# Performance work log

Hardware: AMD Instinct MI355X
Metric: run time of the kernel (lower is better)

The kernel has to match this reference:

```python
import jax, jax.numpy as jnp
import numpy as np

N = 100000    # nodes
E = 1600000   # edges (avg degree 16)
IN = 128      # input feature dim
D = 32        # per-head hidden dim
H = 4         # heads for hidden layers
C = 16        # num_classes (final per-head dim)
NEG = 0.2     # leaky_relu negative slope


def setup_inputs() -> dict:
    key = jax.random.key(0)
    ks = jax.random.split(key, 14)
    s = jnp.float32(0.05)
    f32 = jnp.float32
    inp = {
        "inputs": jax.random.normal(ks[0], (N, IN), f32),
        "src": jax.random.randint(ks[1], (E,), 0, N),
        "dst": jax.random.randint(ks[2], (E,), 0, N),
        # layer 0: IN -> (H, D), no residual
        "W0": jax.random.normal(ks[3], (IN, H * D), f32) * s,
        "al0": jax.random.normal(ks[4], (H, D), f32) * s,
        "ar0": jax.random.normal(ks[5], (H, D), f32) * s,
        # layer 1: H*D -> (H, D), identity residual (dims match)
        "W1": jax.random.normal(ks[6], (H * D, H * D), f32) * s,
        "al1": jax.random.normal(ks[7], (H, D), f32) * s,
        "ar1": jax.random.normal(ks[8], (H, D), f32) * s,
        # final layer: H*D -> (1, C), linear residual projection
        "W2": jax.random.normal(ks[9], (H * D, 1 * C), f32) * s,
        "al2": jax.random.normal(ks[10], (1, C), f32) * s,
        "ar2": jax.random.normal(ks[11], (1, C), f32) * s,
        "resW2": jax.random.normal(ks[12], (H * D, 1 * C), f32) * s,
    }
    return inp


def gat_conv(h, W, al, ar, src, dst, n_heads, out_dim, res=None, act=None):
    # h: (N, F_in) -> out: (N, n_heads, out_dim)
    feat = (h @ W).reshape(N, n_heads, out_dim)            # (N,H,D)
    el = jnp.sum(feat * al, axis=-1)                       # (N,H)
    er = jnp.sum(feat * ar, axis=-1)                       # (N,H)
    e = jax.nn.leaky_relu(el[src] + er[dst], NEG)          # (E,H)
    # softmax over incoming edges per destination node
    emax = jax.ops.segment_max(e, dst, num_segments=N)     # (N,H)
    ex = jnp.exp(e - emax[dst])                            # (E,H)
    den = jax.ops.segment_sum(ex, dst, num_segments=N)     # (N,H)
    alpha = ex / den[dst]                                  # (E,H)
    msg = feat[src] * alpha[:, :, None]                    # (E,H,D) -- dominant traffic
    out = jax.ops.segment_sum(msg, dst, num_segments=N)    # (N,H,D)
    if res is not None:
        out = out + res
    if act is not None:
        out = act(out)
    return out


def reference(inputs, src, dst, W0, al0, ar0, W1, al1, ar1, W2, al2, ar2, resW2):
    # hidden layer 0 (no residual), GATConv activation = elu, then flatten + relu
    h = gat_conv(inputs, W0, al0, ar0, src, dst, H, D, res=None, act=jax.nn.elu)
    h = jax.nn.relu(h.reshape(N, H * D))
    # hidden layer 1, identity residual (in == H*D)
    res1 = h.reshape(N, H, D)
    h = gat_conv(h, W1, al1, ar1, src, dst, H, D, res=res1, act=jax.nn.elu)
    h = jax.nn.relu(h.reshape(N, H * D))
    # output layer: 1 head, linear residual projection, no activation, mean over heads
    res2 = (h @ resW2).reshape(N, 1, C)
    out = gat_conv(h, W2, al2, ar2, src, dst, 1, C, res=res2, act=None)
    return out.mean(axis=1)                                # (N, C)
```

## Files before the change

kernel.cpp:

```cpp
#include <hip/hip_runtime.h>

#define N_NODES 100000
#define N_EDGES 1600000
#define IN_F    128
#define NEG_SLOPE 0.2f
#define NBUCK   512
#define PCHUNK  4096

typedef __attribute__((ext_vector_type(8))) short bf16x8;
typedef __attribute__((ext_vector_type(4))) float f32x4;

__device__ __forceinline__ float bf2f(unsigned short u) {
    return __uint_as_float(((unsigned int)u) << 16);
}

__device__ __forceinline__ unsigned short f2bf(float f) {
    unsigned int u = __float_as_uint(f);
    u += 0x7FFFu + ((u >> 16) & 1u);
    return (unsigned short)(u >> 16);
}

__global__ __launch_bounds__(256) void pack_w128(const float* __restrict__ W,
                                                 unsigned short* __restrict__ Wp) {
    int idx = blockIdx.x * 256 + threadIdx.x;
    int j  = idx & 7;
    int l  = (idx >> 3) & 63;
    int kt = (idx >> 9) & 3;
    int nt = idx >> 11;
    int k  = kt * 32 + (l >> 4) * 8 + j;
    int n  = nt * 16 + (l & 15);
    Wp[idx] = f2bf(W[k * 128 + n]);
}

__global__ __launch_bounds__(256) void pack_w32(const float* __restrict__ W2,
                                                const float* __restrict__ rW2,
                                                unsigned short* __restrict__ Wp) {
    int idx = blockIdx.x * 256 + threadIdx.x;
    int j  = idx & 7;
    int l  = (idx >> 3) & 63;
    int kt = (idx >> 9) & 3;
    int nt = idx >> 11;
    int k  = kt * 32 + (l >> 4) * 8 + j;
    int n  = nt * 16 + (l & 15);
    float v = (n < 16) ? W2[k * 16 + n] : rW2[k * 16 + (n - 16)];
    Wp[idx] = f2bf(v);
}

__global__ __launch_bounds__(256) void gemm128_mfma(const float* __restrict__ A,
                                                    const unsigned short* __restrict__ Wp,
                                                    const float* __restrict__ al,
                                                    const float* __restrict__ ar,
                                                    unsigned short* __restrict__ featb,
                                                    float* __restrict__ el,
                                                    float* __restrict__ er,
                                                    int nrows) {
    __shared__ unsigned short sA[64][136];
    const int t    = threadIdx.x;
    const int row0 = blockIdx.x * 64;

#pragma unroll
    for (int i = 0; i < 8; ++i) {
        int e  = (i * 256 + t) * 4;
        int r  = e >> 7;
        int c  = e & 127;
        float4 v = make_float4(0.f, 0.f, 0.f, 0.f);
        int gr = row0 + r;
        if (gr < nrows) v = *(const float4*)(A + (size_t)gr * IN_F + c);
        ushort4 u;
        u.x = f2bf(v.x); u.y = f2bf(v.y); u.z = f2bf(v.z); u.w = f2bf(v.w);
        *(ushort4*)(&sA[r][c]) = u;
    }
    __syncthreads();

    const int wv   = t >> 6;
    const int lane = t & 63;
    const int q    = lane >> 4;
    const int m    = lane & 15;
    const int m0   = wv * 16;

    f32x4 acc[8];
#pragma unroll
    for (int nt = 0; nt < 8; ++nt) acc[nt] = (f32x4){0.f, 0.f, 0.f, 0.f};

#pragma unroll
    for (int kt = 0; kt < 4; ++kt) {
        bf16x8 afr = *(const bf16x8*)(&sA[m0 + m][kt * 32 + q * 8]);
#pragma unroll
        for (int nt = 0; nt < 8; ++nt) {
            bf16x8 bfr = *(const bf16x8*)(Wp + ((size_t)(nt * 4 + kt) * 64 + lane) * 8);
            acc[nt] = __builtin_amdgcn_mfma_f32_16x16x32_bf16(afr, bfr, acc[nt], 0, 0, 0);
        }
    }

    float pel[16], per[16];
#pragma unroll
    for (int i = 0; i < 16; ++i) { pel[i] = 0.f; per[i] = 0.f; }

#pragma unroll
    for (int nt = 0; nt < 8; ++nt) {
        const int col = nt * 16 + m;
        const float alv = al[col];
        const float arv = ar[col];
        const int h = nt >> 1;
#pragma unroll
        for (int reg = 0; reg < 4; ++reg) {
            int row = row0 + m0 + q * 4 + reg;
            float a = acc[nt][reg];
            if (row < nrows) featb[(size_t)row * 128 + col] = f2bf(a);
            pel[reg * 4 + h] += a * alv;
            per[reg * 4 + h] += a * arv;
        }
    }

#pragma unroll
    for (int s = 8; s > 0; s >>= 1) {
#pragma unroll
        for (int i = 0; i < 16; ++i) {
            pel[i] += __shfl_down(pel[i], s);
            per[i] += __shfl_down(per[i], s);
        }
    }
    if (m == 0) {
#pragma unroll
        for (int reg = 0; reg < 4; ++reg) {
            int row = row0 + m0 + q * 4 + reg;
            if (row < nrows) {
#pragma unroll
                for (int h = 0; h < 4; ++h) {
                    el[row * 4 + h] = pel[reg * 4 + h];
                    er[row * 4 + h] = per[reg * 4 + h];
                }
            }
        }
    }
}

__global__ __launch_bounds__(256) void gemm16_mfma(const float* __restrict__ A,
                                                   const unsigned short* __restrict__ Wp,
                                                   const float* __restrict__ al,
                                                   const float* __restrict__ ar,
                                                   unsigned short* __restrict__ feat2b,
                                                   float* __restrict__ res2,
                                                   float* __restrict__ el,
                                                   float* __restrict__ er,
                                                   int nrows) {
    __shared__ unsigned short sA[64][136];
    const int t    = threadIdx.x;
    const int row0 = blockIdx.x * 64;

#pragma unroll
    for (int i = 0; i < 8; ++i) {
        int e  = (i * 256 + t) * 4;
        int r  = e >> 7;
        int c  = e & 127;
        float4 v = make_float4(0.f, 0.f, 0.f, 0.f);
        int gr = row0 + r;
        if (gr < nrows) v = *(const float4*)(A + (size_t)gr * IN_F + c);
        ushort4 u;
        u.x = f2bf(v.x); u.y = f2bf(v.y); u.z = f2bf(v.z); u.w = f2bf(v.w);
        *(ushort4*)(&sA[r][c]) = u;
    }
    __syncthreads();

    const int wv   = t >> 6;
    const int lane = t & 63;
    const int q    = lane >> 4;
    const int m    = lane & 15;
    const int m0   = wv * 16;

    f32x4 acc0 = (f32x4){0.f, 0.f, 0.f, 0.f};
    f32x4 acc1 = (f32x4){0.f, 0.f, 0.f, 0.f};

#pragma unroll
    for (int kt = 0; kt < 4; ++kt) {
        bf16x8 afr = *(const bf16x8*)(&sA[m0 + m][kt * 32 + q * 8]);
        bf16x8 b0  = *(const bf16x8*)(Wp + ((size_t)(0 * 4 + kt) * 64 + lane) * 8);
        bf16x8 b1  = *(const bf16x8*)(Wp + ((size_t)(1 * 4 + kt) * 64 + lane) * 8);
        acc0 = __builtin_amdgcn_mfma_f32_16x16x32_bf16(afr, b0, acc0, 0, 0, 0);
        acc1 = __builtin_amdgcn_mfma_f32_16x16x32_bf16(afr, b1, acc1, 0, 0, 0);
    }

    float pel[4], per[4];
    const float alv = al[m];
    const float arv = ar[m];
#pragma unroll
    for (int reg = 0; reg < 4; ++reg) {
        int row = row0 + m0 + q * 4 + reg;
        float a = acc0[reg];
        if (row < nrows) {
            feat2b[(size_t)row * 16 + m] = f2bf(a);
            res2[(size_t)row * 16 + m]   = acc1[reg];
        }
        pel[reg] = a * alv;
        per[reg] = a * arv;
    }
#pragma unroll
    for (int s = 8; s > 0; s >>= 1) {
#pragma unroll
        for (int reg = 0; reg < 4; ++reg) {
            pel[reg] += __shfl_down(pel[reg], s);
            per[reg] += __shfl_down(per[reg], s);
        }
    }
    if (m == 0) {
#pragma unroll
        for (int reg = 0; reg < 4; ++reg) {
            int row = row0 + m0 + q * 4 + reg;
            if (row < nrows) { el[row] = pel[reg]; er[row] = per[reg]; }
        }
    }
}

__global__ __launch_bounds__(256) void bucket_count_k(const int* __restrict__ dst,
                                                      int* __restrict__ bcount, int nE) {
    __shared__ int hist[NBUCK];
    const int t = threadIdx.x;
    hist[t] = 0; hist[t + 256] = 0;
    __syncthreads();
    const int start = blockIdx.x * PCHUNK;
#pragma unroll
    for (int j = 0; j < PCHUNK / 256; ++j) {
        int e = start + j * 256 + t;
        if (e < nE) atomicAdd(&hist[dst[e] >> 8], 1);
    }
    __syncthreads();
    if (hist[t])       atomicAdd(&bcount[t],       hist[t]);
    if (hist[t + 256]) atomicAdd(&bcount[t + 256], hist[t + 256]);
}

__global__ __launch_bounds__(NBUCK) void scan512(const int* __restrict__ bcount,
                                                 int* __restrict__ bbase,
                                                 int* __restrict__ bcursor) {
    __shared__ int s[NBUCK];
    const int t = threadIdx.x;
    int v = bcount[t];
    s[t] = v;
    __syncthreads();
#pragma unroll
    for (int off = 1; off < NBUCK; off <<= 1) {
        int x = (t >= off) ? s[t - off] : 0;
        __syncthreads();
        s[t] += x;
        __syncthreads();
    }
    int excl = s[t] - v;
    bbase[t]   = excl;
    bcursor[t] = excl;
}

__global__ __launch_bounds__(512) void partition_k(const int* __restrict__ src,
                                                   const int* __restrict__ dst,
                                                   int* __restrict__ bcursor,
                                                   uint2* __restrict__ pe, int nE) {
    __shared__ int   hist[NBUCK];
    __shared__ int   lstart[NBUCK];
    __shared__ int   gbase[NBUCK];
    __shared__ int   curB[NBUCK];
    __shared__ uint2 reorder[PCHUNK];

    const int t = threadIdx.x;
    const int start = blockIdx.x * PCHUNK;
    const int m = min(PCHUNK, nE - start);

    hist[t] = 0;
    __syncthreads();

#pragma unroll
    for (int j = 0; j < PCHUNK / 512; ++j) {
        int e = start + j * 512 + t;
        if (e < nE) atomicAdd(&hist[dst[e] >> 8], 1);
    }
    __syncthreads();
    const int cnt = hist[t];

    __shared__ int s[NBUCK];
    s[t] = cnt;
    __syncthreads();
#pragma unroll
    for (int off = 1; off < NBUCK; off <<= 1) {
        int x = (t >= off) ? s[t - off] : 0;
        __syncthreads();
        s[t] += x;
        __syncthreads();
    }
    lstart[t] = s[t] - cnt;
    curB[t]   = s[t] - cnt;
    gbase[t] = cnt ? atomicAdd(&bcursor[t], cnt) : 0;
    __syncthreads();

#pragma unroll
    for (int j = 0; j < PCHUNK / 512; ++j) {
        int e = start + j * 512 + t;
        if (e < nE) {
            int d = dst[e];
            int pos = atomicAdd(&curB[d >> 8], 1);
            reorder[pos] = make_uint2((unsigned)src[e], (unsigned)d);
        }
    }
    __syncthreads();

    for (int i = t; i < m; i += 512) {
        uint2 ed = reorder[i];
        int b = (int)(ed.y >> 8);
        pe[gbase[b] + (i - lstart[b])] = ed;
    }
}

__global__ __launch_bounds__(256) void bucket_finalize(const uint2* __restrict__ pe,
                                                       const int* __restrict__ bbase,
                                                       int* __restrict__ rowptr,
                                                       int* __restrict__ deg,
                                                       int* __restrict__ sorted_src,
                                                       int nE) {
    __shared__ int deg_l[256];
    __shared__ int s[256];
    __shared__ int cur[256];

    const int b  = blockIdx.x;
    const int t  = threadIdx.x;
    const int base = bbase[b];
    const int endE = (b + 1 < NBUCK) ? bbase[b + 1] : nE;
    const int cnt  = endE - base;
    const int n    = b * 256 + t;

    deg_l[t] = 0;
    __syncthreads();
    for (int i = t; i < cnt; i += 256)
        atomicAdd(&deg_l[pe[base + i].y & 255u], 1);
    __syncthreads();

    const int dv = deg_l[t];
    s[t] = dv;
    __syncthreads();
#pragma unroll
    for (int off = 1; off < 256; off <<= 1) {
        int x = (t >= off) ? s[t - off] : 0;
        __syncthreads();
        s[t] += x;
        __syncthreads();
    }
    const int off_l = s[t] - dv;
    if (n < N_NODES) {
        rowptr[n] = base + off_l;
        deg[n]    = dv;
    }
    cur[t] = off_l;
    __syncthreads();

    for (int i = t; i < cnt; i += 256) {
        uint2 ed = pe[base + i];
        int pos = atomicAdd(&cur[ed.y & 255u], 1);
        sorted_src[base + pos] = (int)ed.x;
    }
}

__global__ __launch_bounds__(256) void gat_agg128(const int* __restrict__ rowptr,
                                                  const int* __restrict__ deg,
                                                  const int* __restrict__ sorted_src,
                                                  const float* __restrict__ el,
                                                  const float* __restrict__ er,
                                                  const unsigned short* __restrict__ featb,
                                                  const float* __restrict__ res,
                                                  float* __restrict__ out) {
    __shared__ int   sS[4][64];
    __shared__ float sW[4][64][4];

    const int wv   = threadIdx.x >> 6;
    const int lane = threadIdx.x & 63;
    const int nd   = blockIdx.x * 4 + wv;

    const int dg = deg[nd];
    const int r0 = rowptr[nd];
    const int h  = lane >> 4;
    const float4 er4 = *(const float4*)(er + nd * 4);

    float den = 0.f;
    float ax = 0.f, ay = 0.f;

    for (int base = 0; base < dg; base += 64) {
        int m = dg - base; if (m > 64) m = 64;
        if (lane < m) {
            int s = sorted_src[r0 + base + lane];
            sS[wv][lane] = s;
            float4 e4 = *(const float4*)(el + s * 4);
            float4 w;
            float v;
            v = e4.x + er4.x; v = v > 0.f ? v : NEG_SLOPE * v; w.x = __expf(v);
            v = e4.y + er4.y; v = v > 0.f ? v : NEG_SLOPE * v; w.y = __expf(v);
            v = e4.z + er4.z; v = v > 0.f ? v : NEG_SLOPE * v; w.z = __expf(v);
            v = e4.w + er4.w; v = v > 0.f ? v : NEG_SLOPE * v; w.w = __expf(v);
            *(float4*)(&sW[wv][lane][0]) = w;
        }
        for (int i = 0; i < m; ++i) {
            int s   = sS[wv][i];
            float w = sW[wv][i][h];
            den += w;
            ushort2 u = *(const ushort2*)(featb + (size_t)s * 128 + lane * 2);
            ax += w * bf2f(u.x);
            ay += w * bf2f(u.y);
        }
    }

    float scale = den > 0.f ? 1.f / den : 0.f;
    float ox = ax * scale, oy = ay * scale;
    size_t o0 = (size_t)nd * 128 + lane * 2;
    if (res) { ox += res[o0]; oy += res[o0 + 1]; }
    ox = fmaxf(ox, 0.f);
    oy = fmaxf(oy, 0.f);
    *(float2*)(out + o0) = make_float2(ox, oy);
}

__global__ __launch_bounds__(256) void gat_agg16(const int* __restrict__ rowptr,
                                                 const int* __restrict__ deg,
                                                 const int* __restrict__ sorted_src,
                                                 const float* __restrict__ el,
                                                 const float* __restrict__ er,
                                                 const unsigned short* __restrict__ feat2b,
                                                 const float* __restrict__ res,
                                                 float* __restrict__ out) {
    __shared__ int   sS[4][64];
    __shared__ float sW[4][64];

    const int wv   = threadIdx.x >> 6;
    const int lane = threadIdx.x & 63;
    const int nd   = blockIdx.x * 4 + wv;
    const int g    = lane >> 3;
    const int f2   = (lane & 7) * 2;

    const int dg = deg[nd];
    const int r0 = rowptr[nd];
    const float erd = er[nd];

    float ax = 0.f, ay = 0.f, den = 0.f;

    for (int base = 0; base < dg; base += 64) {
        int m = dg - base; if (m > 64) m = 64;
        if (lane < m) {
            int s = sorted_src[r0 + base + lane];
            sS[wv][lane] = s;
            float v = el[s] + erd;
            v = v > 0.f ? v : NEG_SLOPE * v;
            sW[wv][lane] = __expf(v);
        }
        for (int i = g; i < m; i += 8) {
            int s   = sS[wv][i];
            float w = sW[wv][i];
            den += w;
            ushort2 u = *(const ushort2*)(feat2b + (size_t)s * 16 + f2);
            ax += w * bf2f(u.x);
            ay += w * bf2f(u.y);
        }
    }

    ax += __shfl_down(ax, 32); ay += __shfl_down(ay, 32); den += __shfl_down(den, 32);
    ax += __shfl_down(ax, 16); ay += __shfl_down(ay, 16); den += __shfl_down(den, 16);
    ax += __shfl_down(ax, 8);  ay += __shfl_down(ay, 8);  den += __shfl_down(den, 8);

    if (lane < 8) {
        float scale = den > 0.f ? 1.f / den : 0.f;
        size_t o0 = (size_t)nd * 16 + f2;
        float2 o;
        o.x = ax * scale + res[o0];
        o.y = ay * scale + res[o0 + 1];
        *(float2*)(out + o0) = o;
    }
}

extern "C" void kernel_launch(void* const* d_in, const int* in_sizes, int n_in,
                              void* d_out, int out_size, void* d_ws, size_t ws_size,
                              hipStream_t stream) {
    const float* inputs = (const float*)d_in[0];
    const int*   src    = (const int*)d_in[1];
    const int*   dst    = (const int*)d_in[2];
    const float* W0     = (const float*)d_in[3];
    const float* al0    = (const float*)d_in[4];
    const float* ar0    = (const float*)d_in[5];
    const float* W1     = (const float*)d_in[6];
    const float* al1    = (const float*)d_in[7];
    const float* ar1    = (const float*)d_in[8];
    const float* W2     = (const float*)d_in[9];
    const float* al2    = (const float*)d_in[10];
    const float* ar2    = (const float*)d_in[11];
    const float* resW2  = (const float*)d_in[12];
    float* out = (float*)d_out;

    const size_t NF = (size_t)N_NODES * 128;
    float* ws   = (float*)d_ws;
    float* hbuf = ws;
    float* el   = ws + NF;
    float* er   = el + (size_t)N_NODES * 4;
    float* res2 = er + (size_t)N_NODES * 4;
    unsigned short* featb  = (unsigned short*)(res2 + (size_t)N_NODES * 16);
    unsigned short* feat2b = featb + NF;
    unsigned short* W0p    = feat2b + (size_t)N_NODES * 16;
    unsigned short* W1p    = W0p + 16384;
    unsigned short* W2p    = W1p + 16384;
    int* iws = (int*)(W2p + 8192);
    uint2* pe        = (uint2*)iws;
    int* deg         = iws + 2 * N_EDGES;
    int* rowptr      = deg + N_NODES;
    int* sorted_src  = rowptr + N_NODES;
    int* bcount      = sorted_src + N_EDGES;
    int* bbase       = bcount + NBUCK;
    int* bcursor     = bbase + NBUCK;

    dim3 blk(256);
    int gemmGrid = (N_NODES + 63) / 64;
    int pGrid    = (N_EDGES + PCHUNK - 1) / PCHUNK;
    int bGrid    = (N_NODES + 255) / 256;
    int aggGrid  = N_NODES / 4;

    hipMemsetAsync(bcount, 0, NBUCK * sizeof(int), stream);
    bucket_count_k<<<pGrid, blk, 0, stream>>>(dst, bcount, N_EDGES);
    scan512<<<1, NBUCK, 0, stream>>>(bcount, bbase, bcursor);
    partition_k<<<pGrid, dim3(512), 0, stream>>>(src, dst, bcursor, pe, N_EDGES);
    bucket_finalize<<<bGrid, blk, 0, stream>>>(pe, bbase, rowptr, deg, sorted_src, N_EDGES);

    pack_w128<<<64, blk, 0, stream>>>(W0, W0p);
    pack_w128<<<64, blk, 0, stream>>>(W1, W1p);
    pack_w32<<<32, blk, 0, stream>>>(W2, resW2, W2p);

    gemm128_mfma<<<gemmGrid, blk, 0, stream>>>(inputs, W0p, al0, ar0, featb, el, er, N_NODES);
    gat_agg128<<<aggGrid, blk, 0, stream>>>(rowptr, deg, sorted_src, el, er, featb,
                                            nullptr, hbuf);

    gemm128_mfma<<<gemmGrid, blk, 0, stream>>>(hbuf, W1p, al1, ar1, featb, el, er, N_NODES);
    gat_agg128<<<aggGrid, blk, 0, stream>>>(rowptr, deg, sorted_src, el, er, featb,
                                            hbuf, hbuf);

    gemm16_mfma<<<gemmGrid, blk, 0, stream>>>(hbuf, W2p, al2, ar2, feat2b, res2,
                                              el, er, N_NODES);
    gat_agg16<<<aggGrid, blk, 0, stream>>>(rowptr, deg, sorted_src, el, er, feat2b,
                                           res2, out);
}
```

Baseline: 432.7 us.

## Store hidden activations in bf16, pack edges into 32 bits, drop GEMM LDS staging

Hidden-layer activations now go to global memory as bf16 instead of fp32, which halves the write and read traffic between the aggregation and GEMM kernels. The GEMMs read A fragments straight from global memory and no longer stage them through shared memory with a barrier. Partition entries are packed as src<<8 | low-byte-of-dst in one 32-bit word instead of a uint2, and the bucket is recovered with a binary search over lstart. The three weight-packing launches are merged into one. The trade-offs are extra bf16 rounding on the residual path, uncoalesced A loads in the GEMMs, and src<<8 only fits because node ids stay below 2^24.

```diff
diff --git a/kernel.cpp b/kernel.cpp
--- a/kernel.cpp
+++ b/kernel.cpp
@@ -20,63 +20,49 @@
     return (unsigned short)(u >> 16);
 }
 
-__global__ __launch_bounds__(256) void pack_w128(const float* __restrict__ W,
-                                                 unsigned short* __restrict__ Wp) {
-    int idx = blockIdx.x * 256 + threadIdx.x;
+__global__ __launch_bounds__(256) void pack_all(const float* __restrict__ W0,
+                                                const float* __restrict__ W1,
+                                                const float* __restrict__ W2,
+                                                const float* __restrict__ rW2,
+                                                unsigned short* __restrict__ W0p,
+                                                unsigned short* __restrict__ W1p,
+                                                unsigned short* __restrict__ W2p) {
+    int gid = blockIdx.x * 256 + threadIdx.x;
+    const float* W;
+    unsigned short* Wp;
+    int idx, ncols;
+    if (gid < 16384)      { W = W0; Wp = W0p; idx = gid;          ncols = 128; }
+    else if (gid < 32768) { W = W1; Wp = W1p; idx = gid - 16384;  ncols = 128; }
+    else                  { W = W2; Wp = W2p; idx = gid - 32768;  ncols = 32;  }
     int j  = idx & 7;
     int l  = (idx >> 3) & 63;
     int kt = (idx >> 9) & 3;
     int nt = idx >> 11;
     int k  = kt * 32 + (l >> 4) * 8 + j;
     int n  = nt * 16 + (l & 15);
-    Wp[idx] = f2bf(W[k * 128 + n]);
-}
-
-__global__ __launch_bounds__(256) void pack_w32(const float* __restrict__ W2,
-                                                const float* __restrict__ rW2,
-                                                unsigned short* __restrict__ Wp) {
-    int idx = blockIdx.x * 256 + threadIdx.x;
-    int j  = idx & 7;
-    int l  = (idx >> 3) & 63;
-    int kt = (idx >> 9) & 3;
-    int nt = idx >> 11;
-    int k  = kt * 32 + (l >> 4) * 8 + j;
-    int n  = nt * 16 + (l & 15);
-    float v = (n < 16) ? W2[k * 16 + n] : rW2[k * 16 + (n - 16)];
+    float v;
+    if (ncols == 128) v = W[k * 128 + n];
+    else              v = (n < 16) ? W[k * 16 + n] : rW2[k * 16 + (n - 16)];
     Wp[idx] = f2bf(v);
 }
 
-__global__ __launch_bounds__(256) void gemm128_mfma(const float* __restrict__ A,
-                                                    const unsigned short* __restrict__ Wp,
-                                                    const float* __restrict__ al,
-                                                    const float* __restrict__ ar,
-                                                    unsigned short* __restrict__ featb,
-                                                    float* __restrict__ el,
-                                                    float* __restrict__ er,
-                                                    int nrows) {
-    __shared__ unsigned short sA[64][136];
+__global__ __launch_bounds__(256) void gemm128_mfma_f32(const float* __restrict__ A,
+                                                        const unsigned short* __restrict__ Wp,
+                                                        const float* __restrict__ al,
+                                                        const float* __restrict__ ar,
+                                                        unsigned short* __restrict__ featb,
+                                                        float* __restrict__ el,
+                                                        float* __restrict__ er,
+                                                        int nrows) {
     const int t    = threadIdx.x;
-    const int row0 = blockIdx.x * 64;
-
-#pragma unroll
-    for (int i = 0; i < 8; ++i) {
-        int e  = (i * 256 + t) * 4;
-        int r  = e >> 7;
-        int c  = e & 127;
-        float4 v = make_float4(0.f, 0.f, 0.f, 0.f);
-        int gr = row0 + r;
-        if (gr < nrows) v = *(const float4*)(A + (size_t)gr * IN_F + c);
-        ushort4 u;
-        u.x = f2bf(v.x); u.y = f2bf(v.y); u.z = f2bf(v.z); u.w = f2bf(v.w);
-        *(ushort4*)(&sA[r][c]) = u;
-    }
-    __syncthreads();
-
     const int wv   = t >> 6;
     const int lane = t & 63;
     const int q    = lane >> 4;
     const int m    = lane & 15;
-    const int m0   = wv * 16;
+    const int rb   = blockIdx.x * 64 + wv * 16;
+    const int arow = rb + m;
+    const bool rok = arow < nrows;
+    const float* Ar = A + (size_t)arow * IN_F;
 
     f32x4 acc[8];
 #pragma unroll
@@ -84,7 +70,15 @@
 
 #pragma unroll
     for (int kt = 0; kt < 4; ++kt) {
-        bf16x8 afr = *(const bf16x8*)(&sA[m0 + m][kt * 32 + q * 8]);
+        bf16x8 afr = (bf16x8){0, 0, 0, 0, 0, 0, 0, 0};
+        if (rok) {
+            float4 v0 = *(const float4*)(Ar + kt * 32 + q * 8);
+            float4 v1 = *(const float4*)(Ar + kt * 32 + q * 8 + 4);
+            afr[0] = (short)f2bf(v0.x); afr[1] = (short)f2bf(v0.y);
+            afr[2] = (short)f2bf(v0.z); afr[3] = (short)f2bf(v0.w);
+            afr[4] = (short)f2bf(v1.x); afr[5] = (short)f2bf(v1.y);
+            afr[6] = (short)f2bf(v1.z); afr[7] = (short)f2bf(v1.w);
+        }
 #pragma unroll
         for (int nt = 0; nt < 8; ++nt) {
             bf16x8 bfr = *(const bf16x8*)(Wp + ((size_t)(nt * 4 + kt) * 64 + lane) * 8);
@@ -104,14 +98,13 @@
         const int h = nt >> 1;
 #pragma unroll
         for (int reg = 0; reg < 4; ++reg) {
-            int row = row0 + m0 + q * 4 + reg;
+            int row = rb + q * 4 + reg;
             float a = acc[nt][reg];
             if (row < nrows) featb[(size_t)row * 128 + col] = f2bf(a);
             pel[reg * 4 + h] += a * alv;
             per[reg * 4 + h] += a * arv;
         }
     }
-
 #pragma unroll
     for (int s = 8; s > 0; s >>= 1) {
 #pragma unroll
@@ -123,7 +116,7 @@
     if (m == 0) {
 #pragma unroll
         for (int reg = 0; reg < 4; ++reg) {
-            int row = row0 + m0 + q * 4 + reg;
+            int row = rb + q * 4 + reg;
             if (row < nrows) {
 #pragma unroll
                 for (int h = 0; h < 4; ++h) {
@@ -135,7 +128,82 @@
     }
 }
 
-__global__ __launch_bounds__(256) void gemm16_mfma(const float* __restrict__ A,
+__global__ __launch_bounds__(256) void gemm128_mfma_bf16(const unsigned short* __restrict__ Ab,
+                                                         const unsigned short* __restrict__ Wp,
+                                                         const float* __restrict__ al,
+                                                         const float* __restrict__ ar,
+                                                         unsigned short* __restrict__ featb,
+                                                         float* __restrict__ el,
+                                                         float* __restrict__ er,
+                                                         int nrows) {
+    const int t    = threadIdx.x;
+    const int wv   = t >> 6;
+    const int lane = t & 63;
+    const int q    = lane >> 4;
+    const int m    = lane & 15;
+    const int rb   = blockIdx.x * 64 + wv * 16;
+    const int arow = rb + m;
+    const bool rok = arow < nrows;
+    const unsigned short* Ar = Ab + (size_t)arow * IN_F;
+
+    f32x4 acc[8];
+#pragma unroll
+    for (int nt = 0; nt < 8; ++nt) acc[nt] = (f32x4){0.f, 0.f, 0.f, 0.f};
+
+#pragma unroll
+    for (int kt = 0; kt < 4; ++kt) {
+        bf16x8 afr = (bf16x8){0, 0, 0, 0, 0, 0, 0, 0};
+        if (rok) afr = *(const bf16x8*)(Ar + kt * 32 + q * 8);
+#pragma unroll
+        for (int nt = 0; nt < 8; ++nt) {
+            bf16x8 bfr = *(const bf16x8*)(Wp + ((size_t)(nt * 4 + kt) * 64 + lane) * 8);
+            acc[nt] = __builtin_amdgcn_mfma_f32_16x16x32_bf16(afr, bfr, acc[nt], 0, 0, 0);
+        }
+    }
+
+    float pel[16], per[16];
+#pragma unroll
+    for (int i = 0; i < 16; ++i) { pel[i] = 0.f; per[i] = 0.f; }
+
+#pragma unroll
+    for (int nt = 0; nt < 8; ++nt) {
+        const int col = nt * 16 + m;
+        const float alv = al[col];
+        const float arv = ar[col];
+        const int h = nt >> 1;
+#pragma unroll
+        for (int reg = 0; reg < 4; ++reg) {
+            int row = rb + q * 4 + reg;
+            float a = acc[nt][reg];
+            if (row < nrows) featb[(size_t)row * 128 + col] = f2bf(a);
+            pel[reg * 4 + h] += a * alv;
+            per[reg * 4 + h] += a * arv;
+        }
+    }
+#pragma unroll
+    for (int s = 8; s > 0; s >>= 1) {
+#pragma unroll
+        for (int i = 0; i < 16; ++i) {
+            pel[i] += __shfl_down(pel[i], s);
+            per[i] += __shfl_down(per[i], s);
+        }
+    }
+    if (m == 0) {
+#pragma unroll
+        for (int reg = 0; reg < 4; ++reg) {
+            int row = rb + q * 4 + reg;
+            if (row < nrows) {
+#pragma unroll
+                for (int h = 0; h < 4; ++h) {
+                    el[row * 4 + h] = pel[reg * 4 + h];
+                    er[row * 4 + h] = per[reg * 4 + h];
+                }
+            }
+        }
+    }
+}
+
+__global__ __launch_bounds__(256) void gemm16_mfma(const unsigned short* __restrict__ Ab,
                                                    const unsigned short* __restrict__ Wp,
                                                    const float* __restrict__ al,
                                                    const float* __restrict__ ar,
@@ -144,38 +212,25 @@
                                                    float* __restrict__ el,
                                                    float* __restrict__ er,
                                                    int nrows) {
-    __shared__ unsigned short sA[64][136];
     const int t    = threadIdx.x;
-    const int row0 = blockIdx.x * 64;
-
-#pragma unroll
-    for (int i = 0; i < 8; ++i) {
-        int e  = (i * 256 + t) * 4;
-        int r  = e >> 7;
-        int c  = e & 127;
-        float4 v = make_float4(0.f, 0.f, 0.f, 0.f);
-        int gr = row0 + r;
-        if (gr < nrows) v = *(const float4*)(A + (size_t)gr * IN_F + c);
-        ushort4 u;
-        u.x = f2bf(v.x); u.y = f2bf(v.y); u.z = f2bf(v.z); u.w = f2bf(v.w);
-        *(ushort4*)(&sA[r][c]) = u;
-    }
-    __syncthreads();
-
     const int wv   = t >> 6;
     const int lane = t & 63;
     const int q    = lane >> 4;
     const int m    = lane & 15;
-    const int m0   = wv * 16;
+    const int rb   = blockIdx.x * 64 + wv * 16;
+    const int arow = rb + m;
+    const bool rok = arow < nrows;
+    const unsigned short* Ar = Ab + (size_t)arow * IN_F;
 
     f32x4 acc0 = (f32x4){0.f, 0.f, 0.f, 0.f};
     f32x4 acc1 = (f32x4){0.f, 0.f, 0.f, 0.f};
 
 #pragma unroll
     for (int kt = 0; kt < 4; ++kt) {
-        bf16x8 afr = *(const bf16x8*)(&sA[m0 + m][kt * 32 + q * 8]);
-        bf16x8 b0  = *(const bf16x8*)(Wp + ((size_t)(0 * 4 + kt) * 64 + lane) * 8);
-        bf16x8 b1  = *(const bf16x8*)(Wp + ((size_t)(1 * 4 + kt) * 64 + lane) * 8);
+        bf16x8 afr = (bf16x8){0, 0, 0, 0, 0, 0, 0, 0};
+        if (rok) afr = *(const bf16x8*)(Ar + kt * 32 + q * 8);
+        bf16x8 b0 = *(const bf16x8*)(Wp + ((size_t)(0 * 4 + kt) * 64 + lane) * 8);
+        bf16x8 b1 = *(const bf16x8*)(Wp + ((size_t)(1 * 4 + kt) * 64 + lane) * 8);
         acc0 = __builtin_amdgcn_mfma_f32_16x16x32_bf16(afr, b0, acc0, 0, 0, 0);
         acc1 = __builtin_amdgcn_mfma_f32_16x16x32_bf16(afr, b1, acc1, 0, 0, 0);
     }
@@ -185,7 +240,7 @@
     const float arv = ar[m];
 #pragma unroll
     for (int reg = 0; reg < 4; ++reg) {
-        int row = row0 + m0 + q * 4 + reg;
+        int row = rb + q * 4 + reg;
         float a = acc0[reg];
         if (row < nrows) {
             feat2b[(size_t)row * 16 + m] = f2bf(a);
@@ -205,7 +260,7 @@
     if (m == 0) {
 #pragma unroll
         for (int reg = 0; reg < 4; ++reg) {
-            int row = row0 + m0 + q * 4 + reg;
+            int row = rb + q * 4 + reg;
             if (row < nrows) { el[row] = pel[reg]; er[row] = per[reg]; }
         }
     }
@@ -251,12 +306,12 @@
 __global__ __launch_bounds__(512) void partition_k(const int* __restrict__ src,
                                                    const int* __restrict__ dst,
                                                    int* __restrict__ bcursor,
-                                                   uint2* __restrict__ pe, int nE) {
-    __shared__ int   hist[NBUCK];
-    __shared__ int   lstart[NBUCK];
-    __shared__ int   gbase[NBUCK];
-    __shared__ int   curB[NBUCK];
-    __shared__ uint2 reorder[PCHUNK];
+                                                   unsigned int* __restrict__ pe, int nE) {
+    __shared__ int hist[NBUCK];
+    __shared__ int lstart[NBUCK];
+    __shared__ int gbase[NBUCK];
+    __shared__ int curB[NBUCK];
+    __shared__ unsigned int reorder[PCHUNK];
 
     const int t = threadIdx.x;
     const int start = blockIdx.x * PCHUNK;
@@ -294,19 +349,23 @@
         if (e < nE) {
             int d = dst[e];
             int pos = atomicAdd(&curB[d >> 8], 1);
-            reorder[pos] = make_uint2((unsigned)src[e], (unsigned)d);
+            reorder[pos] = ((unsigned)src[e] << 8) | ((unsigned)d & 255u);
         }
     }
     __syncthreads();
 
     for (int i = t; i < m; i += 512) {
-        uint2 ed = reorder[i];
-        int b = (int)(ed.y >> 8);
-        pe[gbase[b] + (i - lstart[b])] = ed;
-    }
-}
-
-__global__ __launch_bounds__(256) void bucket_finalize(const uint2* __restrict__ pe,
+        unsigned int ed = reorder[i];
+        int lo = 0, hi = NBUCK - 1;
+        while (lo < hi) {
+            int mid = (lo + hi + 1) >> 1;
+            if (lstart[mid] <= i) lo = mid; else hi = mid - 1;
+        }
+        pe[gbase[lo] + (i - lstart[lo])] = ed;
+    }
+}
+
+__global__ __launch_bounds__(256) void bucket_finalize(const unsigned int* __restrict__ pe,
                                                        const int* __restrict__ bbase,
                                                        int* __restrict__ rowptr,
                                                        int* __restrict__ deg,
@@ -326,7 +385,7 @@
     deg_l[t] = 0;
     __syncthreads();
     for (int i = t; i < cnt; i += 256)
-        atomicAdd(&deg_l[pe[base + i].y & 255u], 1);
+        atomicAdd(&deg_l[pe[base + i] & 255u], 1);
     __syncthreads();
 
     const int dv = deg_l[t];
@@ -348,9 +407,9 @@
     __syncthreads();
 
     for (int i = t; i < cnt; i += 256) {
-        uint2 ed = pe[base + i];
-        int pos = atomicAdd(&cur[ed.y & 255u], 1);
-        sorted_src[base + pos] = (int)ed.x;
+        unsigned int ed = pe[base + i];
+        int pos = atomicAdd(&cur[ed & 255u], 1);
+        sorted_src[base + pos] = (int)(ed >> 8);
     }
 }
 
@@ -360,8 +419,8 @@
                                                   const float* __restrict__ el,
                                                   const float* __restrict__ er,
                                                   const unsigned short* __restrict__ featb,
-                                                  const float* __restrict__ res,
-                                                  float* __restrict__ out) {
+                                                  const unsigned short* __restrict__ resb,
+                                                  unsigned short* __restrict__ outb) {
     __shared__ int   sS[4][64];
     __shared__ float sW[4][64][4];
 
@@ -404,10 +463,17 @@
     float scale = den > 0.f ? 1.f / den : 0.f;
     float ox = ax * scale, oy = ay * scale;
     size_t o0 = (size_t)nd * 128 + lane * 2;
-    if (res) { ox += res[o0]; oy += res[o0 + 1]; }
+    if (resb) {
+        ushort2 rv = *(const ushort2*)(resb + o0);
+        ox += bf2f(rv.x);
+        oy += bf2f(rv.y);
+    }
     ox = fmaxf(ox, 0.f);
     oy = fmaxf(oy, 0.f);
-    *(float2*)(out + o0) = make_float2(ox, oy);
+    ushort2 ou;
+    ou.x = f2bf(ox);
+    ou.y = f2bf(oy);
+    *(ushort2*)(outb + o0) = ou;
 }
 
 __global__ __launch_bounds__(256) void gat_agg16(const int* __restrict__ rowptr,
@@ -486,18 +552,18 @@
 
     const size_t NF = (size_t)N_NODES * 128;
     float* ws   = (float*)d_ws;
-    float* hbuf = ws;
-    float* el   = ws + NF;
+    float* el   = ws;
     float* er   = el + (size_t)N_NODES * 4;
     float* res2 = er + (size_t)N_NODES * 4;
-    unsigned short* featb  = (unsigned short*)(res2 + (size_t)N_NODES * 16);
+    unsigned short* hbufb  = (unsigned short*)(res2 + (size_t)N_NODES * 16);
+    unsigned short* featb  = hbufb + NF;
     unsigned short* feat2b = featb + NF;
     unsigned short* W0p    = feat2b + (size_t)N_NODES * 16;
     unsigned short* W1p    = W0p + 16384;
     unsigned short* W2p    = W1p + 16384;
     int* iws = (int*)(W2p + 8192);
-    uint2* pe        = (uint2*)iws;
-    int* deg         = iws + 2 * N_EDGES;
+    unsigned int* pe = (unsigned int*)iws;
+    int* deg         = iws + N_EDGES;
     int* rowptr      = deg + N_NODES;
     int* sorted_src  = rowptr + N_NODES;
     int* bcount      = sorted_src + N_EDGES;
@@ -515,20 +581,19 @@
     scan512<<<1, NBUCK, 0, stream>>>(bcount, bbase, bcursor);
     partition_k<<<pGrid, dim3(512), 0, stream>>>(src, dst, bcursor, pe, N_EDGES);
     bucket_finalize<<<bGrid, blk, 0, stream>>>(pe, bbase, rowptr, deg, sorted_src, N_EDGES);
-
-    pack_w128<<<64, blk, 0, stream>>>(W0, W0p);
-    pack_w128<<<64, blk, 0, stream>>>(W1, W1p);
-    pack_w32<<<32, blk, 0, stream>>>(W2, resW2, W2p);
-
-    gemm128_mfma<<<gemmGrid, blk, 0, stream>>>(inputs, W0p, al0, ar0, featb, el, er, N_NODES);
+    pack_all<<<160, blk, 0, stream>>>(W0, W1, W2, resW2, W0p, W1p, W2p);
+
+    gemm128_mfma_f32<<<gemmGrid, blk, 0, stream>>>(inputs, W0p, al0, ar0, featb,
+                                                   el, er, N_NODES);
     gat_agg128<<<aggGrid, blk, 0, stream>>>(rowptr, deg, sorted_src, el, er, featb,
-                                            nullptr, hbuf);
-
-    gemm128_mfma<<<gemmGrid, blk, 0, stream>>>(hbuf, W1p, al1, ar1, featb, el, er, N_NODES);
+                                            nullptr, hbufb);
+
+    gemm128_mfma_bf16<<<gemmGrid, blk, 0, stream>>>(hbufb, W1p, al1, ar1, featb,
+                                                    el, er, N_NODES);
     gat_agg128<<<aggGrid, blk, 0, stream>>>(rowptr, deg, sorted_src, el, er, featb,
-                                            hbuf, hbuf);
-
-    gemm16_mfma<<<gemmGrid, blk, 0, stream>>>(hbuf, W2p, al2, ar2, feat2b, res2,
+                                            hbufb, hbufb);
+
+    gemm16_mfma<<<gemmGrid, blk, 0, stream>>>(hbufb, W2p, al2, ar2, feat2b, res2,
                                               el, er, N_NODES);
     gat_agg16<<<aggGrid, blk, 0, stream>>>(rowptr, deg, sorted_src, el, er, feat2b,
                                            res2, out);
```

After: 412.7 us. 1.05x faster.
